# Performance work log

Hardware: AMD Instinct MI355X
Metric: run time of the kernel (lower is better)

## Reference

```python
import itertools
import jax
import jax.numpy as jnp
import numpy as np

FRAME_H, FRAME_W = 480, 640
HFOV = 79
CAM_H_CM = 88.0
NUM_SEM = 16
MAP_SIZE_CM, RES = 4800, 5
VR = 100
BEEN_CLOSE_CM = 200
GDS = 2
DU = 4
CAT_THR, EXP_THR, MAP_THR = 5.0, 1.0, 1.0
MIN_D_CM, MAX_D_CM = 50.0, 350.0
MIN_OBS_H_CM = 25
DIL_ITER, DIL_SIZE = 1, 3

NON_SEM = 4
LOCAL = MAP_SIZE_CM // GDS // RES
GLOBAL = MAP_SIZE_CM // RES
MAX_VH = int(360 / RES)
MIN_VH = int(-40 / RES)
ZB = MAX_VH - MIN_VH
MIN_Z = int(MIN_OBS_H_CM / RES - MIN_VH)
MAX_Z = int((CAM_H_CM + 1) / RES - MIN_VH)
XC = (FRAME_W - 1) / 2.0
ZC = (FRAME_H - 1) / 2.0
FOCAL = (FRAME_W / 2.0) / np.tan(np.deg2rad(HFOV / 2.0))
DEG = 57.29577951308232
B, T = 2, 4
C_MAP = NON_SEM + NUM_SEM

GPOSE0 = jnp.array([24.0, 24.0, 0.0], jnp.float32)
ORIG0 = jnp.array([12.0, 12.0, 0.0], jnp.float32)
LPOSE0 = GPOSE0 - ORIG0
LMB0 = jnp.array([240, 720, 240, 720], jnp.int32)

_XS = np.arange(FRAME_W, dtype=np.float32)[::DU]
_ZS = np.arange(FRAME_H - 1, -1, -1, dtype=np.float32)[::DU]


def point_cloud(depth):
    d = depth[:, ::DU, ::DU]
    valid = (d > MIN_D_CM) & (d < MAX_D_CM)
    X = (_XS[None, None, :] - XC) * d / FOCAL
    Z = (_ZS[None, :, None] - ZC) * d / FOCAL
    pts = jnp.stack([X, d, Z], -1).reshape(d.shape[0], -1, 3)
    return pts, valid.reshape(d.shape[0], -1)


def avg_pool(x, k):
    b, c, h, w = x.shape
    return x.reshape(b, c, h // k, k, w // k, k).mean((3, 5))


def splat(feat, coords):
    bs, fc, n = feat.shape
    dims = (VR, VR, ZB)
    G = VR * VR * ZB
    pos = [coords[:, d] * dims[d] / 2.0 + dims[d] / 2.0 for d in range(3)]
    fl = [jnp.floor(p) for p in pos]
    out = jnp.zeros((fc, bs * G), feat.dtype)
    offs = (jnp.arange(bs) * G)[:, None]
    for corner in itertools.product((0.0, 1.0), repeat=3):
        idx = jnp.zeros_like(pos[0])
        w = jnp.ones_like(pos[0])
        for d in range(3):
            p = fl[d] + corner[d]
            safe = ((p > 0) & (p < dims[d])).astype(feat.dtype)
            w = w * (1.0 - jnp.abs(pos[d] - p)) * safe
            idx = idx * dims[d] + p * safe
        flat = (idx.astype(jnp.int32) + offs).reshape(-1)
        vals = (feat * w[:, None, :]).transpose(1, 0, 2).reshape(fc, -1)
        out = out.at[:, flat].add(vals)
    out = jnp.round(out)
    return out.reshape(fc, bs, VR, VR, ZB).transpose(1, 0, 2, 3, 4)


def affine_grid(theta, h, w):
    ys = jnp.linspace(-1.0, 1.0, h)
    xs = jnp.linspace(-1.0, 1.0, w)
    gy, gx = jnp.meshgrid(ys, xs, indexing="ij")
    base = jnp.stack([gx, gy, jnp.ones_like(gx)], -1)
    return jnp.einsum("bij,hwj->bhwi", theta, base)


def _sample_one(im, grid):
    c, h, w = im.shape
    x = (grid[..., 0] + 1.0) * (w - 1) / 2.0
    y = (grid[..., 1] + 1.0) * (h - 1) / 2.0
    x0 = jnp.floor(x)
    y0 = jnp.floor(y)
    out = jnp.zeros((c,) + x.shape, im.dtype)
    for dx, dy in ((0, 0), (1, 0), (0, 1), (1, 1)):
        xi = x0 + dx
        yi = y0 + dy
        wgt = (1.0 - jnp.abs(x - xi)) * (1.0 - jnp.abs(y - yi))
        ok = (xi >= 0) & (xi <= w - 1) & (yi >= 0) & (yi <= h - 1)
        xi_c = jnp.clip(xi, 0, w - 1).astype(jnp.int32)
        yi_c = jnp.clip(yi, 0, h - 1).astype(jnp.int32)
        out = out + im[:, yi_c, xi_c] * (wgt * ok)[None]
    return out


grid_sample = jax.vmap(_sample_one)


def get_new_pose(pose, rel):
    s = jnp.sin(pose[:, 2] / DEG)
    c = jnp.cos(pose[:, 2] / DEG)
    x = pose[:, 0] + rel[:, 0] * c - rel[:, 1] * s
    y = pose[:, 1] + rel[:, 0] * s + rel[:, 1] * c
    o = pose[:, 2] + rel[:, 2] * DEG
    o = jnp.fmod(o - 180.0, 360.0) + 180.0
    o = jnp.fmod(o + 180.0, 360.0) - 180.0
    return jnp.stack([x, y, o], 1)


def update_local(obs, pdelta, prev_map, prev_pose):
    bs = obs.shape[0]
    pts, valid = point_cloud(obs[:, 3])
    pts = pts.at[..., 2].add(CAM_H_CM)
    pts = pts.at[..., 0].add(VR * RES / 2.0)
    cx = (pts[..., 0] / RES - VR // 2) / VR * 2.0
    cy = (pts[..., 1] / RES - VR // 2) / VR * 2.0
    cz = (pts[..., 2] / RES - (MAX_VH + MIN_VH) // 2) / ZB * 2.0
    coords = jnp.stack([cx, cy, cz], 1)
    coords = jnp.where(valid[:, None, :], coords, 2.0)
    sem = avg_pool(obs[:, 4:], DU).reshape(bs, NUM_SEM, -1)
    feat = jnp.concatenate([jnp.ones_like(sem[:, :1]), sem], 1)
    vox = splat(feat, coords)
    agent_h = vox[..., MIN_Z:MAX_Z].sum(-1)
    all_h = vox.sum(-1)
    fp_map = jnp.clip(agent_h[:, :1] / MAP_THR, 0.0, 1.0)
    fp_exp = jnp.clip(all_h[:, :1] / EXP_THR, 0.0, 1.0)
    sem_pred = jnp.clip(agent_h[:, 1:] / CAT_THR, 0.0, 1.0)
    x1 = LOCAL // 2 - VR // 2
    y1 = LOCAL // 2
    av = jnp.zeros((bs, C_MAP, LOCAL, LOCAL), obs.dtype)
    av = av.at[:, 0:1, y1:y1 + VR, x1:x1 + VR].set(fp_map)
    av = av.at[:, 1:2, y1:y1 + VR, x1:x1 + VR].set(fp_exp)
    av = av.at[:, NON_SEM:, y1:y1 + VR, x1:x1 + VR].set(sem_pred)
    pose = get_new_pose(prev_pose, pdelta)
    half = LOCAL // 2
    stx = -(pose[:, 0] * 100.0 / RES - half) / half
    sty = -(pose[:, 1] * 100.0 / RES - half) / half
    th = (90.0 - pose[:, 2]) * (np.pi / 180.0)
    ct, snt = jnp.cos(th), jnp.sin(th)
    zr, on = jnp.zeros_like(ct), jnp.ones_like(ct)
    th1 = jnp.stack([jnp.stack([ct, -snt, zr], -1), jnp.stack([snt, ct, zr], -1)], 1)
    th2 = jnp.stack([jnp.stack([on, zr, stx], -1), jnp.stack([zr, on, sty], -1)], 1)
    rotated = grid_sample(av, affine_grid(th1, LOCAL, LOCAL))
    translated = grid_sample(rotated, affine_grid(th2, LOCAL, LOCAL))
    cur = jnp.maximum(prev_map, translated)
    obst = cur[:, 0:1]
    kern = jnp.ones((1, 1, DIL_SIZE, DIL_SIZE), cur.dtype)
    for _ in range(DIL_ITER):
        obst = (jax.lax.conv(obst, kern, (1, 1), "SAME") > 0.5).astype(cur.dtype)
    cur = cur.at[:, 0].set(obst[:, 0])
    xg = (pose[:, 0] * 100.0 / RES).astype(jnp.int32)
    yg = (pose[:, 1] * 100.0 / RES).astype(jnp.int32)
    rr = jnp.arange(LOCAL)
    drow = rr[None, :, None] - yg[:, None, None]
    dcol = rr[None, None, :] - xg[:, None, None]
    sq = ((jnp.abs(drow) <= 2) & (jnp.abs(dcol) <= 2)).astype(cur.dtype)
    cur = cur.at[:, 2].set(sq)
    rad = BEEN_CLOSE_CM // RES
    disk = ((drow * drow + dcol * dcol) <= rad * rad).astype(cur.dtype)
    cur = cur.at[:, 3].set(jnp.maximum(cur[:, 3], disk))
    return cur, pose


def update_global_env(lmap, gmap, lpose, gpose, lmb, orig, updg):
    gpose_n = lpose + orig
    gmap_n = jax.lax.dynamic_update_slice(gmap, lmap, (0, lmb[0], lmb[2]))
    r = (gpose_n[1] * 100.0 / RES).astype(jnp.int32)
    c = (gpose_n[0] * 100.0 / RES).astype(jnp.int32)
    gx1 = jnp.clip(r - LOCAL // 2, 0, GLOBAL - LOCAL)
    gy1 = jnp.clip(c - LOCAL // 2, 0, GLOBAL - LOCAL)
    lmb_n = jnp.stack([gx1, gx1 + LOCAL, gy1, gy1 + LOCAL]).astype(jnp.int32)
    orig_n = jnp.stack([gy1 * RES / 100.0, gx1 * RES / 100.0, jnp.zeros(())]).astype(orig.dtype)
    lmap_n = jax.lax.dynamic_slice(gmap_n, (0, lmb_n[0], lmb_n[2]), lmap.shape)
    lpose_n = gpose_n - orig_n
    w = lambda a, b: jnp.where(updg, a, b)
    return (w(lmap_n, lmap), w(gmap_n, gmap), w(lpose_n, lpose),
            w(gpose_n, gpose), w(lmb_n, lmb), w(orig_n, orig))


def map_features(lmap, gmap):
    bs = gmap.shape[0]
    gdown = gmap[:, :NON_SEM].reshape(bs, NON_SEM, LOCAL, GDS, LOCAL, GDS).max((3, 5))
    return jnp.concatenate([lmap[:, :NON_SEM], gdown, lmap[:, NON_SEM:]], 1)


def forward(seq_obs, seq_pose_delta, seq_dones, seq_update_global, seq_camera_poses,
            init_local_map, init_global_map, init_local_pose, init_global_pose,
            init_lmb, init_origins):
    def step(carry, xs):
        lmap, gmap, lpose, gpose, lmb, orig = carry
        obs, pdelta, done, updg = xs
        d4 = done[:, None, None, None]
        d2 = done[:, None]
        lmap = jnp.where(d4, 0.0, lmap)
        gmap = jnp.where(d4, 0.0, gmap)
        lpose = jnp.where(d2, LPOSE0, lpose)
        gpose = jnp.where(d2, GPOSE0, gpose)
        lmb = jnp.where(d2, LMB0, lmb)
        orig = jnp.where(d2, ORIG0, orig)
        lmap, lpose = update_local(obs, pdelta, lmap, lpose)
        lmap, gmap, lpose, gpose, lmb, orig = jax.vmap(update_global_env)(
            lmap, gmap, lpose, gpose, lmb, orig, updg)
        feats = map_features(lmap, gmap)
        return (lmap, gmap, lpose, gpose, lmb, orig), (feats, lpose, gpose, lmb, orig)

    carry0 = (init_local_map, init_global_map, init_local_pose, init_global_pose,
              init_lmb, init_origins)
    xs = (jnp.swapaxes(seq_obs, 0, 1), jnp.swapaxes(seq_pose_delta, 0, 1),
          jnp.swapaxes(seq_dones, 0, 1), jnp.swapaxes(seq_update_global, 0, 1))
    (lmap, gmap, _, _, _, _), (fe, lp, gp, lb, og) = jax.lax.scan(step, carry0, xs)
    sw = lambda a: jnp.swapaxes(a, 0, 1)
    return sw(fe), lmap, gmap, sw(lp), sw(gp), sw(lb), sw(og)


def setup_inputs() -> dict:
    key = jax.random.key(0)
    ks = jax.random.split(key, 4)
    rgb = jax.random.uniform(ks[0], (B, T, 3, FRAME_H, FRAME_W), jnp.float32)
    depth = MIN_D_CM + jax.random.uniform(ks[1], (B, T, 1, FRAME_H, FRAME_W), jnp.float32) * (MAX_D_CM - MIN_D_CM + 100.0)
    seg = (jax.random.uniform(ks[2], (B, T, NUM_SEM, FRAME_H, FRAME_W)) > 0.95).astype(jnp.float32)
    seq_obs = jnp.concatenate([rgb, depth, seg], 2)
    seq_pose_delta = jax.random.normal(ks[3], (B, T, 3), jnp.float32) * jnp.array([0.25, 0.05, 0.1], jnp.float32)
    return {
        "seq_obs": seq_obs,
        "seq_pose_delta": seq_pose_delta,
        "seq_dones": jnp.zeros((B, T), bool),
        "seq_update_global": jnp.ones((B, T), bool),
        "seq_camera_poses": jnp.tile(jnp.eye(4, dtype=jnp.float32)[None], (B, 1, 1)),
        "init_local_map": jnp.zeros((B, C_MAP, LOCAL, LOCAL), jnp.float32),
        "init_global_map": jnp.zeros((B, C_MAP, GLOBAL, GLOBAL), jnp.float32),
        "init_local_pose": jnp.tile(LPOSE0[None], (B, 1)),
        "init_global_pose": jnp.tile(GPOSE0[None], (B, 1)),
        "init_lmb": jnp.tile(LMB0[None], (B, 1)),
        "init_origins": jnp.tile(ORIG0[None], (B, 1)),
    }


def reference(seq_obs, seq_pose_delta, seq_dones, seq_update_global, seq_camera_poses,
              init_local_map, init_global_map, init_local_pose, init_global_pose,
              init_lmb, init_origins):
    return forward(seq_obs, seq_pose_delta, seq_dones, seq_update_global, seq_camera_poses,
                   init_local_map, init_global_map, init_local_pose, init_global_pose,
                   init_lmb, init_origins)
```

## Files before the change

kernel.cpp:

```cpp
#include <hip/hip_runtime.h>
#include <math.h>


#define BB 2
#define TT 4
#define CMAP 20
#define LOC 480
#define GLOB 960
#define VOXC 17
#define NH 120
#define NW 160
#define NPTS (NH*NW)
#define LOC2 (LOC*LOC)
#define G2 (GLOB*GLOB)
#define FH 480
#define FW 640
#define LOCW 240
#define LOCW2 (LOCW*LOCW)
#define WOFF 120
#define CH0Z 69
#define SEMZ 12
#define CELLS 6100
#define CHSZ ((CH0Z + 16*SEMZ)*CELLS)

#define FE_OFF 0L
#define LM_OFF 44236800L
#define LM_SZ  9216000L
#define GM_OFF 53452800L
#define GM_SZ  36864000L
#define LP_OFF 90316800L
#define GP_OFF 90316824L
#define LB_OFF 90316848L
#define OG_OFF 90316880L

#define VOX_SZ   (2L*CHSZ)
#define RED_OFF  3184200L
#define ROT_OFF  3544200L
#define TMP_OFF  5617800L
#define CUR_OFF  6078600L
#define PTF_OFF  15294600L
#define PTI_OFF  15294664L
#define GLIN_OFF 15294728L

__device__ __forceinline__ int iabs(int v){ return v<0? -v : v; }

__global__ __launch_bounds__(256) void k_init0(float4* __restrict__ vox,
                                               float4* __restrict__ lmap,
                                               float4* __restrict__ gmap){
    const long NV4 = VOX_SZ/4;
    const long L4  = LM_SZ/4;
    const long G4  = GM_SZ/4;
    const long total = NV4+L4+G4;
    float4 z; z.x=0.f;z.y=0.f;z.z=0.f;z.w=0.f;
    long i = (long)blockIdx.x*blockDim.x + threadIdx.x;
    long st = (long)gridDim.x*blockDim.x;
    for(long k=i;k<total;k+=st){
        if(k<NV4) vox[k]=z;
        else if(k<NV4+L4) lmap[k-NV4]=z;
        else gmap[k-NV4-L4]=z;
    }
}

__global__ void k_poses(const float* __restrict__ ilp,const float* __restrict__ igp,
                        const int* __restrict__ ilmb,const float* __restrict__ iog,
                        const unsigned char* __restrict__ dones_raw,
                        const unsigned char* __restrict__ updg_raw,
                        const float* __restrict__ pdelta,
                        float* __restrict__ out,float* __restrict__ ptf,int* __restrict__ pti,
                        float* __restrict__ glin){
    #pragma clang fp contract(off)
    int tid = threadIdx.x;
    if(tid < LOC){
        float g;
        if(tid==LOC-1) g = 1.0f;
        else { float s = (float)tid/479.0f; g = s - (1.0f - s); }
        glin[tid] = g;
    }
    if(tid!=0 || blockIdx.x!=0) return;
    int stride;
    if(updg_raw[1]|updg_raw[2]|updg_raw[3]) stride = 1;
    else if(updg_raw[4])                    stride = 4;
    else                                    stride = 8;
    const float DEGF = 57.29577951308232f;
    for(int b=0;b<BB;b++){
        float lp0=ilp[b*3],lp1=ilp[b*3+1],lp2=ilp[b*3+2];
        float gp0=igp[b*3],gp1=igp[b*3+1],gp2=igp[b*3+2];
        float og0=iog[b*3],og1=iog[b*3+1],og2=iog[b*3+2];
        int m0=ilmb[b*4],m1=ilmb[b*4+1],m2=ilmb[b*4+2],m3=ilmb[b*4+3];
        for(int t=0;t<TT;t++){
            int dn = dones_raw[(b*TT+t)*stride]!=0;
            int ug = updg_raw[(b*TT+t)*stride]!=0;
            if(dn){
                lp0=12.f;lp1=12.f;lp2=0.f; gp0=24.f;gp1=24.f;gp2=0.f;
                og0=12.f;og1=12.f;og2=0.f; m0=240;m1=720;m2=240;m3=720;
            }
            float r0=pdelta[(b*TT+t)*3+0], r1=pdelta[(b*TT+t)*3+1], r2=pdelta[(b*TT+t)*3+2];
            float s=sinf(lp2/DEGF), c=cosf(lp2/DEGF);
            float x = lp0 + r0*c - r1*s;
            float y = lp1 + r0*s + r1*c;
            float o = lp2 + r2*DEGF;
            o = fmodf(o-180.f,360.f)+180.f;
            o = fmodf(o+180.f,360.f)-180.f;
            lp0=x; lp1=y; lp2=o;
            float th = (90.0f - o) * (float)(M_PI/180.0);
            float ct = cosf(th), snt = sinf(th);
            float ax = (lp0*100.0f)/5.0f;
            float ay = (lp1*100.0f)/5.0f;
            float stx = -((ax-240.0f)/240.0f);
            float sty = -((ay-240.0f)/240.0f);
            float* pf = ptf + (size_t)(t*BB+b)*8;
            pf[0]=lp0; pf[1]=lp1; pf[2]=o; pf[3]=ct; pf[4]=snt; pf[5]=stx; pf[6]=sty;
            int* pi = pti + (size_t)(t*BB+b)*8;
            pi[0]=m0; pi[1]=m2;
            pi[4]=(int)ax; pi[5]=(int)ay;
            pi[6]=dn; pi[7]=ug;
            float g0=lp0+og0, g1=lp1+og1, g2=lp2+og2;
            if(ug){
                int r  = (int)((g1*100.0f)/5.0f);
                int cc = (int)((g0*100.0f)/5.0f);
                int gx1 = min(max(r-240,0),480);
                int gy1 = min(max(cc-240,0),480);
                m0=gx1; m1=gx1+480; m2=gy1; m3=gy1+480;
                float o0 = ((float)gy1*5.0f)/100.0f;
                float o1 = ((float)gx1*5.0f)/100.0f;
                og0=o0; og1=o1; og2=0.f;
                lp0=g0-o0; lp1=g1-o1; lp2=g2;
                gp0=g0; gp1=g1; gp2=g2;
            }
            pi[2]=m0; pi[3]=m2;
            out[LP_OFF+(b*TT+t)*3+0]=lp0; out[LP_OFF+(b*TT+t)*3+1]=lp1; out[LP_OFF+(b*TT+t)*3+2]=lp2;
            out[GP_OFF+(b*TT+t)*3+0]=gp0; out[GP_OFF+(b*TT+t)*3+1]=gp1; out[GP_OFF+(b*TT+t)*3+2]=gp2;
            out[OG_OFF+(b*TT+t)*3+0]=og0; out[OG_OFF+(b*TT+t)*3+1]=og1; out[OG_OFF+(b*TT+t)*3+2]=og2;
            out[LB_OFF+(b*TT+t)*4+0]=(float)m0; out[LB_OFF+(b*TT+t)*4+1]=(float)m1;
            out[LB_OFF+(b*TT+t)*4+2]=(float)m2; out[LB_OFF+(b*TT+t)*4+3]=(float)m3;
        }
    }
}

__global__ __launch_bounds__(256) void k_reset_done(float4* __restrict__ lmap,float4* __restrict__ gmap,
                                                    const int* __restrict__ pti,int t){
    const long L4 = (long)CMAP*LOC2/4, G4 = (long)CMAP*G2/4, per = L4+G4;
    bool d0 = pti[(size_t)(t*BB+0)*8+6]!=0, d1 = pti[(size_t)(t*BB+1)*8+6]!=0;
    long total = (d0?per:0)+(d1?per:0);
    if(total==0) return;
    float4 z; z.x=0.f;z.y=0.f;z.z=0.f;z.w=0.f;
    long i = (long)blockIdx.x*blockDim.x + threadIdx.x;
    long st = (long)gridDim.x*blockDim.x;
    for(long k=i;k<total;k+=st){
        long r = k; int b;
        if(d0){ if(r<per) b=0; else { b=1; r-=per; } } else b=1;
        if(r<L4) lmap[b*L4+r]=z; else gmap[b*G4+(r-L4)]=z;
    }
}

__global__ __launch_bounds__(256) void k_splat(const float* __restrict__ obs,int t,
                                               float* __restrict__ vox,float FOCAL){
    #pragma clang fp contract(off)
    int tid = blockIdx.x*blockDim.x + threadIdx.x;
    if(tid >= BB*VOXC*NPTS) return;
    int p  = tid % NPTS;
    int ch = (tid/NPTS) % VOXC;
    int b  = tid / (VOXC*NPTS);
    int zi = p / NW, xi = p % NW;
    const float* ob = obs + ((size_t)(b*TT+t))*CMAP*FH*FW;
    float d = ob[3*FH*FW + (size_t)(4*zi)*FW + 4*xi];
    if(!(d>50.0f && d<350.0f)) return;
    float f;
    if(ch==0) f = 1.0f;
    else{
        const float* cp = ob + (size_t)(4+ch-1)*FH*FW + (size_t)(4*zi)*FW + 4*xi;
        float s=0.f;
        #pragma unroll
        for(int r=0;r<4;r++){
            float4 v = *(const float4*)(cp + (size_t)r*FW);
            s += v.x+v.y+v.z+v.w;
        }
        f = s*0.0625f;
    }
    float X  = ((float)(4*xi) - 319.5f)*d/FOCAL;
    float Zc = ((float)(479-4*zi) - 239.5f)*d/FOCAL;
    float p0f = X + 250.0f;
    float p1f = d;
    float p2f = Zc + 88.0f;
    float cx = (p0f/5.0f - 50.0f)/100.0f*2.0f;
    float cy = (p1f/5.0f - 50.0f)/100.0f*2.0f;
    float cz = (p2f/5.0f - 32.0f)/80.0f*2.0f;
    float pos0 = cx*100.0f/2.0f + 50.0f;
    float pos1 = cy*100.0f/2.0f + 50.0f;
    float pos2 = cz*80.0f/2.0f + 40.0f;
    float f0=floorf(pos0), f1=floorf(pos1), f2=floorf(pos2);
    float* base = vox + (size_t)b*CHSZ;
    #pragma unroll
    for(int c0=0;c0<2;c0++){
        float q0=f0+(float)c0;
        if(!(q0>0.f && q0<100.f)) continue;
        float w0 = 1.0f-fabsf(pos0-q0);
        int iq0 = (int)q0;
        #pragma unroll
        for(int c1=0;c1<2;c1++){
            float q1=f1+(float)c1;
            if(!(q1>=10.0f && q1<=70.0f)) continue;
            float w1 = w0*(1.0f-fabsf(pos1-q1));
            int cell = iq0*61 + ((int)q1-10);
            #pragma unroll
            for(int c2=0;c2<2;c2++){
                float q2=f2+(float)c2;
                if(!(q2>0.f && q2<70.f)) continue;
                int iq2 = (int)q2;
                float w = w1*(1.0f-fabsf(pos2-q2));
                if(ch==0)
                    atomicAdd(base + (size_t)(iq2-1)*CELLS + cell, w);
                else if(iq2>=13 && iq2<25)
                    atomicAdd(base + (size_t)(CH0Z + (ch-1)*SEMZ + (iq2-13))*CELLS + cell, f*w);
            }
        }
    }
}

__global__ __launch_bounds__(256) void k_reduce(float* __restrict__ vox,float* __restrict__ red){
    int tid = blockIdx.x*blockDim.x + threadIdx.x;
    if(tid >= BB*VOXC*10000) return;
    int cell = tid % 10000;
    int ch   = (tid/10000) % VOXC;
    int b    = tid / (VOXC*10000);
    int q0 = cell/100, q1 = cell%100;
    float allh=0.f, ag=0.f;
    if(q1>=10 && q1<=70){
        float* base = vox + (size_t)b*CHSZ;
        if(ch==0){
            float* vp = base + q0*61 + (q1-10);
            for(int z=0;z<CH0Z;z++){
                float v = rintf(vp[(size_t)z*CELLS]);
                allh += v;
                if(z>=12 && z<24) ag += v;
                vp[(size_t)z*CELLS] = 0.0f;
            }
        }else{
            float* vp = base + (size_t)(CH0Z + (ch-1)*SEMZ)*CELLS + q0*61 + (q1-10);
            for(int z=0;z<SEMZ;z++){
                float v = rintf(vp[(size_t)z*CELLS]);
                ag += v;
                vp[(size_t)z*CELLS] = 0.0f;
            }
        }
    }
    float* rb = red + (size_t)b*18*10000;
    if(ch==0){
        rb[cell]       = fminf(fmaxf(ag,0.f),1.f);
        rb[10000+cell] = fminf(fmaxf(allh,0.f),1.f);
    }else{
        rb[(ch+1)*10000+cell] = fminf(fmaxf(ag/5.0f,0.f),1.f);
    }
}

__global__ __launch_bounds__(256) void k_rot(const float* __restrict__ red,const float* __restrict__ ptf,
                                             const float* __restrict__ glin,int t,
                                             float* __restrict__ rotW){
    #pragma clang fp contract(off)
    int tid = blockIdx.x*blockDim.x + threadIdx.x;
    if(tid >= BB*LOCW2) return;
    int wx = tid % LOCW;
    int wy = (tid/LOCW) % LOCW;
    int b  = tid / LOCW2;
    int x = wx + WOFF, y = wy + WOFF;
    const float* pf = ptf + (size_t)(t*BB+b)*8;
    float ct = pf[3], snt = pf[4];
    float gx = glin[x], gy = glin[y];
    float grx = ct*gx - snt*gy;
    float gry = snt*gx + ct*gy;
    float xs = (grx+1.0f)*239.5f;
    float ys = (gry+1.0f)*239.5f;
    float x0 = floorf(xs), y0 = floorf(ys);
    int   off[4]; float w[4];
    #pragma unroll
    for(int k=0;k<4;k++){
        float xi = x0 + (float)(k&1), yi = y0 + (float)(k>>1);
        float wgt = (1.0f-fabsf(xs-xi))*(1.0f-fabsf(ys-yi));
        int xii=(int)xi, yii=(int)yi;
        bool ok = !(xi<0.f||xi>479.f||yi<0.f||yi>479.f)
                  && yii>=240 && yii<340 && xii>=190 && xii<290;
        w[k]   = ok ? wgt : 0.0f;
        off[k] = ok ? (yii-240)*100 + (xii-190) : 0;
    }
    const float* rb = red + (size_t)b*18*10000;
    float* rp = rotW + (size_t)b*18*LOCW2 + (size_t)wy*LOCW + wx;
    for(int ch=0;ch<18;ch++){
        const float* rc = rb + (size_t)ch*10000;
        float acc = rc[off[0]]*w[0];
        acc += rc[off[1]]*w[1];
        acc += rc[off[2]]*w[2];
        acc += rc[off[3]]*w[3];
        rp[(size_t)ch*LOCW2] = acc;
    }
}

__global__ __launch_bounds__(256) void k_trans(const float* __restrict__ rotW,const float* __restrict__ ptf,
                                               const int* __restrict__ pti,const float* __restrict__ glin,
                                               int t,const float* __restrict__ P,
                                               float* __restrict__ C,float* __restrict__ tmp0){
    #pragma clang fp contract(off)
    int tid = blockIdx.x*blockDim.x + threadIdx.x;
    if(tid >= BB*LOC2) return;
    int x = tid % LOC;
    int y = (tid/LOC) % LOC;
    int b = tid / LOC2;
    const float* pf = ptf + (size_t)(t*BB+b)*8;
    const int*   pi = pti + (size_t)(t*BB+b)*8;
    float stx = pf[5], sty = pf[6];
    float xs = (glin[x]+stx+1.0f)*239.5f;
    float ys = (glin[y]+sty+1.0f)*239.5f;
    float x0=floorf(xs), y0=floorf(ys);
    int   off[4]; float w[4];
    #pragma unroll
    for(int k=0;k<4;k++){
        float xi = x0 + (float)(k&1), yi = y0 + (float)(k>>1);
        float wgt = (1.0f-fabsf(xs-xi))*(1.0f-fabsf(ys-yi));
        int xii=(int)xi, yii=(int)yi;
        bool ok = !(xi<0.f||xi>479.f||yi<0.f||yi>479.f)
                  && xii>=WOFF && xii<WOFF+LOCW && yii>=WOFF && yii<WOFF+LOCW;
        w[k]   = ok ? wgt : 0.0f;
        off[k] = ok ? (yii-WOFF)*LOCW + (xii-WOFF) : 0;
    }
    int xg=pi[4], yg=pi[5];
    float sq   = (iabs(y-yg)<=2 && iabs(x-xg)<=2) ? 1.0f : 0.0f;
    int dr=y-yg, dc=x-xg;
    float disk = (dr*dr+dc*dc <= 1600) ? 1.0f : 0.0f;
    const float* rb = rotW + (size_t)b*18*LOCW2;
    size_t pix = (size_t)y*LOC + x;
    const float* Pb = P + (size_t)b*CMAP*LOC2 + pix;
    float* Cb = C + (size_t)b*CMAP*LOC2 + pix;
    for(int c=0;c<CMAP;c++){
        if(c==2){ Cb[2*LOC2] = sq; continue; }
        if(c==3){ Cb[3*LOC2] = fmaxf(Pb[3*LOC2], disk); continue; }
        int wc = (c<2) ? c : c-2;
        const float* rp = rb + (size_t)wc*LOCW2;
        float acc = rp[off[0]]*w[0];
        acc += rp[off[1]]*w[1];
        acc += rp[off[2]]*w[2];
        acc += rp[off[3]]*w[3];
        float res = fmaxf(Pb[(size_t)c*LOC2], acc);
        if(c==0) tmp0[(size_t)b*LOC2 + pix] = res;
        else     Cb[(size_t)c*LOC2] = res;
    }
}

__global__ __launch_bounds__(256) void k_dil(const float* __restrict__ tmp0,float* __restrict__ C){
    int tid = blockIdx.x*blockDim.x + threadIdx.x;
    if(tid >= BB*LOC2) return;
    int x = tid % LOC;
    int y = (tid/LOC) % LOC;
    int b = tid / LOC2;
    const float* tb = tmp0 + (size_t)b*LOC2;
    float s=0.f;
    for(int dy=-1;dy<=1;dy++){
        int yy=y+dy; if(yy<0||yy>=LOC) continue;
        for(int dx=-1;dx<=1;dx++){
            int xx=x+dx; if(xx<0||xx>=LOC) continue;
            s += tb[(size_t)yy*LOC+xx];
        }
    }
    C[(size_t)b*CMAP*LOC2 + (size_t)y*LOC + x] = (s>0.5f)?1.0f:0.0f;
}

__global__ __launch_bounds__(256) void k_out(const float* __restrict__ C,float* __restrict__ gmap,
                                             float* __restrict__ P,float* __restrict__ fe,
                                             const int* __restrict__ pti,int t){
    int tid = blockIdx.x*blockDim.x + threadIdx.x;
    if(tid >= BB*LOC2) return;
    int x = tid % LOC;
    int y = (tid/LOC) % LOC;
    int b = tid / LOC2;
    const int* pi = pti + (size_t)(t*BB+b)*8;
    int r0o=pi[0], c0o=pi[1], r0n=pi[2], c0n=pi[3];
    int ug = pi[7];
    size_t pix = (size_t)y*LOC + x;
    const float* Cb = C + (size_t)b*CMAP*LOC2;
    float* gB = gmap + (size_t)b*CMAP*G2;
    float* pB = P + (size_t)b*CMAP*LOC2;
    float* feB = fe + ((size_t)(b*TT+t))*24*LOC2;
    if(ug){
        size_t gp = (size_t)(r0o+y)*GLOB + (c0o+x);
        for(int c=0;c<CMAP;c++)
            gB[(size_t)c*G2 + gp] = Cb[(size_t)c*LOC2 + pix];
    }
    int dr = ug ? (r0n - r0o) : 0;
    int dc = ug ? (c0n - c0o) : 0;
    int sy = y + dr, sx = x + dc;
    bool inT = (sy>=0 && sy<LOC && sx>=0 && sx<LOC);
    size_t gpn = ug ? ((size_t)(r0n+y)*GLOB + (c0n+x)) : 0;
    size_t spix = (size_t)sy*LOC + sx;
    for(int c=0;c<CMAP;c++){
        float v = inT ? Cb[(size_t)c*LOC2 + spix]
                      : gB[(size_t)c*G2 + gpn];
        pB[(size_t)c*LOC2 + pix] = v;
        int fc = (c<4) ? c : c+4;
        feB[(size_t)fc*LOC2 + pix] = v;
    }
    for(int gc=0;gc<4;gc++){
        float m = 0.f; bool first = true;
        #pragma unroll
        for(int dy=0;dy<2;dy++){
            #pragma unroll
            for(int dx=0;dx<2;dx++){
                int ty = 2*y+dy, tx = 2*x+dx;
                int ly = ty - r0o, lx = tx - c0o;
                float tv;
                if(ug && ly>=0 && ly<LOC && lx>=0 && lx<LOC)
                    tv = Cb[(size_t)gc*LOC2 + (size_t)ly*LOC + lx];
                else
                    tv = gB[(size_t)gc*G2 + (size_t)ty*GLOB + tx];
                m = first ? tv : fmaxf(m, tv);
                first = false;
            }
        }
        feB[(size_t)(4+gc)*LOC2 + pix] = m;
    }
}

extern "C" void kernel_launch(void* const* d_in, const int* in_sizes, int n_in,
                              void* d_out, int out_size, void* d_ws, size_t ws_size,
                              hipStream_t stream){
    const float* obs    = (const float*)d_in[0];
    const float* pdelta = (const float*)d_in[1];
    const unsigned char* dones_raw = (const unsigned char*)d_in[2];
    const unsigned char* updg_raw  = (const unsigned char*)d_in[3];
    const float* ilp  = (const float*)d_in[7];
    const float* igp  = (const float*)d_in[8];
    const int*   ilmb = (const int*)d_in[9];
    const float* iog  = (const float*)d_in[10];

    float* out  = (float*)d_out;
    float* fe   = out + FE_OFF;
    float* lmap = out + LM_OFF;
    float* gmap = out + GM_OFF;

    float* ws   = (float*)d_ws;
    float* vox  = ws;
    float* red  = ws + RED_OFF;
    float* rotW = ws + ROT_OFF;
    float* tmp0 = ws + TMP_OFF;
    float* curm = ws + CUR_OFF;
    float* ptf  = ws + PTF_OFF;
    int*   pti  = (int*)(ws + PTI_OFF);
    float* glin = ws + GLIN_OFF;

    const float FOCAL = (float)(320.0 / tan(39.5 * M_PI / 180.0));

    k_init0<<<2048,256,0,stream>>>((float4*)vox,(float4*)lmap,(float4*)gmap);
    k_poses<<<1,512,0,stream>>>(ilp,igp,ilmb,iog,dones_raw,updg_raw,pdelta,out,ptf,pti,glin);

    for(int t=0;t<TT;t++){
        k_reset_done<<<2048,256,0,stream>>>((float4*)lmap,(float4*)gmap,pti,t);
        { int n=BB*VOXC*NPTS;   k_splat <<<(n+255)/256,256,0,stream>>>(obs,t,vox,FOCAL); }
        { int n=BB*VOXC*10000;  k_reduce<<<(n+255)/256,256,0,stream>>>(vox,red); }
        { int n=BB*LOCW2;       k_rot   <<<(n+255)/256,256,0,stream>>>(red,ptf,glin,t,rotW); }
        { int n=BB*LOC2;        k_trans <<<(n+255)/256,256,0,stream>>>(rotW,ptf,pti,glin,t,lmap,curm,tmp0); }
        { int n=BB*LOC2;        k_dil   <<<(n+255)/256,256,0,stream>>>(tmp0,curm); }
        { int n=BB*LOC2;        k_out   <<<(n+255)/256,256,0,stream>>>(curm,gmap,lmap,fe,pti,t); }
    }
}
```

Baseline: 1.093 ms.

## Fuse rotate into translate, dilation into output, and overlap next-step splat/reduce

The separate rotation pass and its intermediate buffer are removed: each translate thread recomputes the rotated bilinear samples of its four source cells straight from the reduced grid. Dilation is evaluated on the fly inside the output kernel instead of in its own pass. The next timestep's splat and reduce are folded into the translate and output kernels, and init is merged with pose computation, which cuts the number of launches. In exchange, the translate kernel does about four times more gathers, dilation is recomputed several times per pixel, and the reduce step inside the output kernel both reads and clears the shared voxel/reduced buffers while the same launch is running. That in-kernel reduce also writes the reduced grid that the translate step reads, so ordering depends on the launch sequence.

Result: faster. 1.065 ms (-2.6%).

```diff
diff --git a/kernel.cpp b/kernel.cpp
--- a/kernel.cpp
+++ b/kernel.cpp
@@ -35,48 +35,29 @@
 
 #define VOX_SZ   (2L*CHSZ)
 #define RED_OFF  3184200L
-#define ROT_OFF  3544200L
-#define TMP_OFF  5617800L
-#define CUR_OFF  6078600L
-#define PTF_OFF  15294600L
-#define PTI_OFF  15294664L
-#define GLIN_OFF 15294728L
+#define TMP_OFF  3544200L
+#define CUR_OFF  4005000L
+#define PTF_OFF  13221000L
+#define PTI_OFF  13221064L
+#define GLIN_OFF 13221128L
 
 __device__ __forceinline__ int iabs(int v){ return v<0? -v : v; }
 
-__global__ __launch_bounds__(256) void k_init0(float4* __restrict__ vox,
-                                               float4* __restrict__ lmap,
-                                               float4* __restrict__ gmap){
-    const long NV4 = VOX_SZ/4;
-    const long L4  = LM_SZ/4;
-    const long G4  = GM_SZ/4;
-    const long total = NV4+L4+G4;
-    float4 z; z.x=0.f;z.y=0.f;z.z=0.f;z.w=0.f;
-    long i = (long)blockIdx.x*blockDim.x + threadIdx.x;
-    long st = (long)gridDim.x*blockDim.x;
-    for(long k=i;k<total;k+=st){
-        if(k<NV4) vox[k]=z;
-        else if(k<NV4+L4) lmap[k-NV4]=z;
-        else gmap[k-NV4-L4]=z;
-    }
-}
-
-__global__ void k_poses(const float* __restrict__ ilp,const float* __restrict__ igp,
-                        const int* __restrict__ ilmb,const float* __restrict__ iog,
-                        const unsigned char* __restrict__ dones_raw,
-                        const unsigned char* __restrict__ updg_raw,
-                        const float* __restrict__ pdelta,
-                        float* __restrict__ out,float* __restrict__ ptf,int* __restrict__ pti,
-                        float* __restrict__ glin){
+
+__device__ __forceinline__ void glin_body(int i, float* glin){
+    float g;
+    if(i==LOC-1) g = 1.0f;
+    else { float s = (float)i/479.0f; g = s - (1.0f - s); }
+    glin[i] = g;
+}
+
+__device__ void poses_body(const float* ilp,const float* igp,
+                           const int* ilmb,const float* iog,
+                           const unsigned char* dones_raw,
+                           const unsigned char* updg_raw,
+                           const float* pdelta,
+                           float* out,float* ptf,int* pti){
     #pragma clang fp contract(off)
-    int tid = threadIdx.x;
-    if(tid < LOC){
-        float g;
-        if(tid==LOC-1) g = 1.0f;
-        else { float s = (float)tid/479.0f; g = s - (1.0f - s); }
-        glin[tid] = g;
-    }
-    if(tid!=0 || blockIdx.x!=0) return;
     int stride;
     if(updg_raw[1]|updg_raw[2]|updg_raw[3]) stride = 1;
     else if(updg_raw[4])                    stride = 4;
@@ -137,27 +118,9 @@
     }
 }
 
-__global__ __launch_bounds__(256) void k_reset_done(float4* __restrict__ lmap,float4* __restrict__ gmap,
-                                                    const int* __restrict__ pti,int t){
-    const long L4 = (long)CMAP*LOC2/4, G4 = (long)CMAP*G2/4, per = L4+G4;
-    bool d0 = pti[(size_t)(t*BB+0)*8+6]!=0, d1 = pti[(size_t)(t*BB+1)*8+6]!=0;
-    long total = (d0?per:0)+(d1?per:0);
-    if(total==0) return;
-    float4 z; z.x=0.f;z.y=0.f;z.z=0.f;z.w=0.f;
-    long i = (long)blockIdx.x*blockDim.x + threadIdx.x;
-    long st = (long)gridDim.x*blockDim.x;
-    for(long k=i;k<total;k+=st){
-        long r = k; int b;
-        if(d0){ if(r<per) b=0; else { b=1; r-=per; } } else b=1;
-        if(r<L4) lmap[b*L4+r]=z; else gmap[b*G4+(r-L4)]=z;
-    }
-}
-
-__global__ __launch_bounds__(256) void k_splat(const float* __restrict__ obs,int t,
-                                               float* __restrict__ vox,float FOCAL){
+__device__ __forceinline__ void splat_body(int tid,const float* __restrict__ obs,int t,
+                                           float* __restrict__ vox,float FOCAL){
     #pragma clang fp contract(off)
-    int tid = blockIdx.x*blockDim.x + threadIdx.x;
-    if(tid >= BB*VOXC*NPTS) return;
     int p  = tid % NPTS;
     int ch = (tid/NPTS) % VOXC;
     int b  = tid / (VOXC*NPTS);
@@ -217,9 +180,7 @@
     }
 }
 
-__global__ __launch_bounds__(256) void k_reduce(float* __restrict__ vox,float* __restrict__ red){
-    int tid = blockIdx.x*blockDim.x + threadIdx.x;
-    if(tid >= BB*VOXC*10000) return;
+__device__ __forceinline__ void reduce_body(int tid,float* __restrict__ vox,float* __restrict__ red){
     int cell = tid % 10000;
     int ch   = (tid/10000) % VOXC;
     int b    = tid / (VOXC*10000);
@@ -253,64 +214,22 @@
     }
 }
 
-__global__ __launch_bounds__(256) void k_rot(const float* __restrict__ red,const float* __restrict__ ptf,
-                                             const float* __restrict__ glin,int t,
-                                             float* __restrict__ rotW){
+__device__ void transf_body(int tid,const float* __restrict__ red,
+                            const float* __restrict__ ptf,const int* __restrict__ pti,
+                            const float* __restrict__ glin,int t,
+                            const float* __restrict__ P,
+                            float* __restrict__ C,float* __restrict__ tmp0){
     #pragma clang fp contract(off)
-    int tid = blockIdx.x*blockDim.x + threadIdx.x;
-    if(tid >= BB*LOCW2) return;
-    int wx = tid % LOCW;
-    int wy = (tid/LOCW) % LOCW;
-    int b  = tid / LOCW2;
-    int x = wx + WOFF, y = wy + WOFF;
-    const float* pf = ptf + (size_t)(t*BB+b)*8;
-    float ct = pf[3], snt = pf[4];
-    float gx = glin[x], gy = glin[y];
-    float grx = ct*gx - snt*gy;
-    float gry = snt*gx + ct*gy;
-    float xs = (grx+1.0f)*239.5f;
-    float ys = (gry+1.0f)*239.5f;
-    float x0 = floorf(xs), y0 = floorf(ys);
-    int   off[4]; float w[4];
-    #pragma unroll
-    for(int k=0;k<4;k++){
-        float xi = x0 + (float)(k&1), yi = y0 + (float)(k>>1);
-        float wgt = (1.0f-fabsf(xs-xi))*(1.0f-fabsf(ys-yi));
-        int xii=(int)xi, yii=(int)yi;
-        bool ok = !(xi<0.f||xi>479.f||yi<0.f||yi>479.f)
-                  && yii>=240 && yii<340 && xii>=190 && xii<290;
-        w[k]   = ok ? wgt : 0.0f;
-        off[k] = ok ? (yii-240)*100 + (xii-190) : 0;
-    }
-    const float* rb = red + (size_t)b*18*10000;
-    float* rp = rotW + (size_t)b*18*LOCW2 + (size_t)wy*LOCW + wx;
-    for(int ch=0;ch<18;ch++){
-        const float* rc = rb + (size_t)ch*10000;
-        float acc = rc[off[0]]*w[0];
-        acc += rc[off[1]]*w[1];
-        acc += rc[off[2]]*w[2];
-        acc += rc[off[3]]*w[3];
-        rp[(size_t)ch*LOCW2] = acc;
-    }
-}
-
-__global__ __launch_bounds__(256) void k_trans(const float* __restrict__ rotW,const float* __restrict__ ptf,
-                                               const int* __restrict__ pti,const float* __restrict__ glin,
-                                               int t,const float* __restrict__ P,
-                                               float* __restrict__ C,float* __restrict__ tmp0){
-    #pragma clang fp contract(off)
-    int tid = blockIdx.x*blockDim.x + threadIdx.x;
-    if(tid >= BB*LOC2) return;
     int x = tid % LOC;
     int y = (tid/LOC) % LOC;
     int b = tid / LOC2;
     const float* pf = ptf + (size_t)(t*BB+b)*8;
     const int*   pi = pti + (size_t)(t*BB+b)*8;
-    float stx = pf[5], sty = pf[6];
+    float ct = pf[3], snt = pf[4], stx = pf[5], sty = pf[6];
     float xs = (glin[x]+stx+1.0f)*239.5f;
     float ys = (glin[y]+sty+1.0f)*239.5f;
     float x0=floorf(xs), y0=floorf(ys);
-    int   off[4]; float w[4];
+    float tw[4]; int ro[4][4]; float rw[4][4];
     #pragma unroll
     for(int k=0;k<4;k++){
         float xi = x0 + (float)(k&1), yi = y0 + (float)(k>>1);
@@ -318,14 +237,34 @@
         int xii=(int)xi, yii=(int)yi;
         bool ok = !(xi<0.f||xi>479.f||yi<0.f||yi>479.f)
                   && xii>=WOFF && xii<WOFF+LOCW && yii>=WOFF && yii<WOFF+LOCW;
-        w[k]   = ok ? wgt : 0.0f;
-        off[k] = ok ? (yii-WOFF)*LOCW + (xii-WOFF) : 0;
+        tw[k] = ok ? wgt : 0.0f;
+        if(ok){
+            float gx2 = glin[xii], gy2 = glin[yii];
+            float grx = ct*gx2 - snt*gy2;
+            float gry = snt*gx2 + ct*gy2;
+            float rxs = (grx+1.0f)*239.5f;
+            float rys = (gry+1.0f)*239.5f;
+            float rx0 = floorf(rxs), ry0 = floorf(rys);
+            #pragma unroll
+            for(int j=0;j<4;j++){
+                float xj = rx0 + (float)(j&1), yj = ry0 + (float)(j>>1);
+                float rwgt = (1.0f-fabsf(rxs-xj))*(1.0f-fabsf(rys-yj));
+                int xjj=(int)xj, yjj=(int)yj;
+                bool okj = !(xj<0.f||xj>479.f||yj<0.f||yj>479.f)
+                           && yjj>=240 && yjj<340 && xjj>=190 && xjj<290;
+                rw[k][j] = okj ? rwgt : 0.0f;
+                ro[k][j] = okj ? (yjj-240)*100 + (xjj-190) : 0;
+            }
+        }else{
+            #pragma unroll
+            for(int j=0;j<4;j++){ rw[k][j]=0.0f; ro[k][j]=0; }
+        }
     }
     int xg=pi[4], yg=pi[5];
     float sq   = (iabs(y-yg)<=2 && iabs(x-xg)<=2) ? 1.0f : 0.0f;
     int dr=y-yg, dc=x-xg;
     float disk = (dr*dr+dc*dc <= 1600) ? 1.0f : 0.0f;
-    const float* rb = rotW + (size_t)b*18*LOCW2;
+    const float* rb = red + (size_t)b*18*10000;
     size_t pix = (size_t)y*LOC + x;
     const float* Pb = P + (size_t)b*CMAP*LOC2 + pix;
     float* Cb = C + (size_t)b*CMAP*LOC2 + pix;
@@ -333,24 +272,23 @@
         if(c==2){ Cb[2*LOC2] = sq; continue; }
         if(c==3){ Cb[3*LOC2] = fmaxf(Pb[3*LOC2], disk); continue; }
         int wc = (c<2) ? c : c-2;
-        const float* rp = rb + (size_t)wc*LOCW2;
-        float acc = rp[off[0]]*w[0];
-        acc += rp[off[1]]*w[1];
-        acc += rp[off[2]]*w[2];
-        acc += rp[off[3]]*w[3];
+        const float* rc = rb + (size_t)wc*10000;
+        float rv0 = rc[ro[0][0]]*rw[0][0]; rv0 += rc[ro[0][1]]*rw[0][1];
+        rv0 += rc[ro[0][2]]*rw[0][2];      rv0 += rc[ro[0][3]]*rw[0][3];
+        float rv1 = rc[ro[1][0]]*rw[1][0]; rv1 += rc[ro[1][1]]*rw[1][1];
+        rv1 += rc[ro[1][2]]*rw[1][2];      rv1 += rc[ro[1][3]]*rw[1][3];
+        float rv2 = rc[ro[2][0]]*rw[2][0]; rv2 += rc[ro[2][1]]*rw[2][1];
+        rv2 += rc[ro[2][2]]*rw[2][2];      rv2 += rc[ro[2][3]]*rw[2][3];
+        float rv3 = rc[ro[3][0]]*rw[3][0]; rv3 += rc[ro[3][1]]*rw[3][1];
+        rv3 += rc[ro[3][2]]*rw[3][2];      rv3 += rc[ro[3][3]]*rw[3][3];
+        float acc = rv0*tw[0]; acc += rv1*tw[1]; acc += rv2*tw[2]; acc += rv3*tw[3];
         float res = fmaxf(Pb[(size_t)c*LOC2], acc);
         if(c==0) tmp0[(size_t)b*LOC2 + pix] = res;
         else     Cb[(size_t)c*LOC2] = res;
     }
 }
 
-__global__ __launch_bounds__(256) void k_dil(const float* __restrict__ tmp0,float* __restrict__ C){
-    int tid = blockIdx.x*blockDim.x + threadIdx.x;
-    if(tid >= BB*LOC2) return;
-    int x = tid % LOC;
-    int y = (tid/LOC) % LOC;
-    int b = tid / LOC2;
-    const float* tb = tmp0 + (size_t)b*LOC2;
+__device__ __forceinline__ float dil_at(const float* __restrict__ tb,int y,int x){
     float s=0.f;
     for(int dy=-1;dy<=1;dy++){
         int yy=y+dy; if(yy<0||yy>=LOC) continue;
@@ -359,14 +297,12 @@
             s += tb[(size_t)yy*LOC+xx];
         }
     }
-    C[(size_t)b*CMAP*LOC2 + (size_t)y*LOC + x] = (s>0.5f)?1.0f:0.0f;
-}
-
-__global__ __launch_bounds__(256) void k_out(const float* __restrict__ C,float* __restrict__ gmap,
-                                             float* __restrict__ P,float* __restrict__ fe,
-                                             const int* __restrict__ pti,int t){
-    int tid = blockIdx.x*blockDim.x + threadIdx.x;
-    if(tid >= BB*LOC2) return;
+    return (s>0.5f)?1.0f:0.0f;
+}
+
+__device__ void outf_body(int tid,const float* __restrict__ C,const float* __restrict__ tmp0,
+                          float* __restrict__ gmap,float* __restrict__ P,float* __restrict__ fe,
+                          const int* __restrict__ pti,int t){
     int x = tid % LOC;
     int y = (tid/LOC) % LOC;
     int b = tid / LOC2;
@@ -375,12 +311,14 @@
     int ug = pi[7];
     size_t pix = (size_t)y*LOC + x;
     const float* Cb = C + (size_t)b*CMAP*LOC2;
+    const float* tb = tmp0 + (size_t)b*LOC2;
     float* gB = gmap + (size_t)b*CMAP*G2;
     float* pB = P + (size_t)b*CMAP*LOC2;
     float* feB = fe + ((size_t)(b*TT+t))*24*LOC2;
     if(ug){
         size_t gp = (size_t)(r0o+y)*GLOB + (c0o+x);
-        for(int c=0;c<CMAP;c++)
+        gB[gp] = dil_at(tb,y,x);
+        for(int c=1;c<CMAP;c++)
             gB[(size_t)c*G2 + gp] = Cb[(size_t)c*LOC2 + pix];
     }
     int dr = ug ? (r0n - r0o) : 0;
@@ -390,8 +328,9 @@
     size_t gpn = ug ? ((size_t)(r0n+y)*GLOB + (c0n+x)) : 0;
     size_t spix = (size_t)sy*LOC + sx;
     for(int c=0;c<CMAP;c++){
-        float v = inT ? Cb[(size_t)c*LOC2 + spix]
-                      : gB[(size_t)c*G2 + gpn];
+        float v;
+        if(inT) v = (c==0) ? dil_at(tb,sy,sx) : Cb[(size_t)c*LOC2 + spix];
+        else    v = gB[(size_t)c*G2 + gpn];
         pB[(size_t)c*LOC2 + pix] = v;
         int fc = (c<4) ? c : c+4;
         feB[(size_t)fc*LOC2 + pix] = v;
@@ -406,7 +345,8 @@
                 int ly = ty - r0o, lx = tx - c0o;
                 float tv;
                 if(ug && ly>=0 && ly<LOC && lx>=0 && lx<LOC)
-                    tv = Cb[(size_t)gc*LOC2 + (size_t)ly*LOC + lx];
+                    tv = (gc==0) ? dil_at(tb,ly,lx)
+                                 : Cb[(size_t)gc*LOC2 + (size_t)ly*LOC + lx];
                 else
                     tv = gB[(size_t)gc*G2 + (size_t)ty*GLOB + tx];
                 m = first ? tv : fmaxf(m, tv);
@@ -415,6 +355,88 @@
         }
         feB[(size_t)(4+gc)*LOC2 + pix] = m;
     }
+}
+
+
+__global__ __launch_bounds__(256) void k_init(float4* __restrict__ vox,
+                                              float4* __restrict__ lmap,float4* __restrict__ gmap,
+                                              const float* ilp,const float* igp,
+                                              const int* ilmb,const float* iog,
+                                              const unsigned char* dones_raw,const unsigned char* updg_raw,
+                                              const float* pdelta,float* out,
+                                              float* ptf,int* pti,float* glin){
+    long i = (long)blockIdx.x*blockDim.x + threadIdx.x;
+    if(blockIdx.x==0){
+        if(threadIdx.x < LOC) glin_body((int)threadIdx.x, glin);
+        if(threadIdx.x == 0)
+            poses_body(ilp,igp,ilmb,iog,dones_raw,updg_raw,pdelta,out,ptf,pti);
+    }
+    const long NV4 = VOX_SZ/4, L4 = LM_SZ/4, G4 = GM_SZ/4;
+    const long total = NV4+L4+G4;
+    float4 z; z.x=0.f;z.y=0.f;z.z=0.f;z.w=0.f;
+    long st = (long)gridDim.x*blockDim.x;
+    for(long k=i;k<total;k+=st){
+        if(k<NV4) vox[k]=z;
+        else if(k<NV4+L4) lmap[k-NV4]=z;
+        else gmap[k-NV4-L4]=z;
+    }
+}
+
+__global__ __launch_bounds__(256) void k_reset(float4* __restrict__ lmap,float4* __restrict__ gmap,
+                                               const int* __restrict__ pti,int t){
+    const long L4 = (long)CMAP*LOC2/4, G4 = (long)CMAP*G2/4, per = L4+G4;
+    bool d0 = pti[(size_t)(t*BB+0)*8+6]!=0, d1 = pti[(size_t)(t*BB+1)*8+6]!=0;
+    long total = (d0?per:0)+(d1?per:0);
+    if(total==0) return;
+    float4 z; z.x=0.f;z.y=0.f;z.z=0.f;z.w=0.f;
+    long i = (long)blockIdx.x*blockDim.x + threadIdx.x;
+    long st = (long)gridDim.x*blockDim.x;
+    for(long k=i;k<total;k+=st){
+        long r = k; int b;
+        if(d0){ if(r<per) b=0; else { b=1; r-=per; } } else b=1;
+        if(r<L4) lmap[b*L4+r]=z; else gmap[b*G4+(r-L4)]=z;
+    }
+}
+
+__global__ __launch_bounds__(256) void k_splat(const float* __restrict__ obs,int t,
+                                               float* __restrict__ vox,float FOCAL){
+    int tid = blockIdx.x*blockDim.x + threadIdx.x;
+    if(tid >= BB*VOXC*NPTS) return;
+    splat_body(tid,obs,t,vox,FOCAL);
+}
+
+__global__ __launch_bounds__(256) void k_reduce(float* __restrict__ vox,float* __restrict__ red){
+    int tid = blockIdx.x*blockDim.x + threadIdx.x;
+    if(tid >= BB*VOXC*10000) return;
+    reduce_body(tid,vox,red);
+}
+
+__global__ __launch_bounds__(256) void k_transf(const float* __restrict__ red,
+                                                const float* __restrict__ ptf,const int* __restrict__ pti,
+                                                const float* __restrict__ glin,int t,
+                                                const float* __restrict__ P,
+                                                float* __restrict__ C,float* __restrict__ tmp0,
+                                                const float* __restrict__ obs,
+                                                float* __restrict__ vox,float FOCAL,int tnext){
+    int NT  = (int)(gridDim.x*blockDim.x);
+    int tid = (int)(blockIdx.x*blockDim.x + threadIdx.x);
+    if(tnext>=0)
+        for(int i=tid;i<BB*VOXC*NPTS;i+=NT) splat_body(i,obs,tnext,vox,FOCAL);
+    if(tid >= BB*LOC2) return;
+    transf_body(tid,red,ptf,pti,glin,t,P,C,tmp0);
+}
+
+__global__ __launch_bounds__(256) void k_outf(const float* __restrict__ C,const float* __restrict__ tmp0,
+                                              float* __restrict__ gmap,float* __restrict__ P,
+                                              float* __restrict__ fe,
+                                              const int* __restrict__ pti,int t,
+                                              float* __restrict__ vox,float* __restrict__ red,int tnext){
+    int NT  = (int)(gridDim.x*blockDim.x);
+    int tid = (int)(blockIdx.x*blockDim.x + threadIdx.x);
+    if(tnext>=0)
+        for(int i=tid;i<BB*VOXC*10000;i+=NT) reduce_body(i,vox,red);
+    if(tid >= BB*LOC2) return;
+    outf_body(tid,C,tmp0,gmap,P,fe,pti,t);
 }
 
 extern "C" void kernel_launch(void* const* d_in, const int* in_sizes, int n_in,
@@ -434,28 +456,30 @@
     float* lmap = out + LM_OFF;
     float* gmap = out + GM_OFF;
 
-    float* ws   = (float*)d_ws;
-    float* vox  = ws;
-    float* red  = ws + RED_OFF;
-    float* rotW = ws + ROT_OFF;
-    float* tmp0 = ws + TMP_OFF;
-    float* curm = ws + CUR_OFF;
-    float* ptf  = ws + PTF_OFF;
-    int*   pti  = (int*)(ws + PTI_OFF);
-    float* glin = ws + GLIN_OFF;
+    float* wsf  = (float*)d_ws;
+    float* vox  = wsf;
+    float* red  = wsf + RED_OFF;
+    float* tmp0 = wsf + TMP_OFF;
+    float* curm = wsf + CUR_OFF;
+    float* ptf  = wsf + PTF_OFF;
+    int*   pti  = (int*)(wsf + PTI_OFF);
+    float* glin = wsf + GLIN_OFF;
 
     const float FOCAL = (float)(320.0 / tan(39.5 * M_PI / 180.0));
 
-    k_init0<<<2048,256,0,stream>>>((float4*)vox,(float4*)lmap,(float4*)gmap);
-    k_poses<<<1,512,0,stream>>>(ilp,igp,ilmb,iog,dones_raw,updg_raw,pdelta,out,ptf,pti,glin);
-
+    k_init<<<2048,256,0,stream>>>((float4*)vox,(float4*)lmap,(float4*)gmap,
+                                  ilp,igp,ilmb,iog,dones_raw,updg_raw,pdelta,
+                                  out,ptf,pti,glin);
+    { int n=BB*VOXC*NPTS;  k_splat <<<(n+255)/256,256,0,stream>>>(obs,0,vox,FOCAL); }
+    { int n=BB*VOXC*10000; k_reduce<<<(n+255)/256,256,0,stream>>>(vox,red); }
+
+    const int nPix = BB*LOC2;
     for(int t=0;t<TT;t++){
-        k_reset_done<<<2048,256,0,stream>>>((float4*)lmap,(float4*)gmap,pti,t);
-        { int n=BB*VOXC*NPTS;   k_splat <<<(n+255)/256,256,0,stream>>>(obs,t,vox,FOCAL); }
-        { int n=BB*VOXC*10000;  k_reduce<<<(n+255)/256,256,0,stream>>>(vox,red); }
-        { int n=BB*LOCW2;       k_rot   <<<(n+255)/256,256,0,stream>>>(red,ptf,glin,t,rotW); }
-        { int n=BB*LOC2;        k_trans <<<(n+255)/256,256,0,stream>>>(rotW,ptf,pti,glin,t,lmap,curm,tmp0); }
-        { int n=BB*LOC2;        k_dil   <<<(n+255)/256,256,0,stream>>>(tmp0,curm); }
-        { int n=BB*LOC2;        k_out   <<<(n+255)/256,256,0,stream>>>(curm,gmap,lmap,fe,pti,t); }
-    }
-}
+        k_reset<<<2048,256,0,stream>>>((float4*)lmap,(float4*)gmap,pti,t);
+        int tnext = (t+1<TT) ? t+1 : -1;
+        k_transf<<<nPix/256,256,0,stream>>>(red,ptf,pti,glin,t,lmap,curm,tmp0,
+                                            obs,vox,FOCAL,tnext);
+        k_outf  <<<nPix/256,256,0,stream>>>(curm,tmp0,gmap,lmap,fe,pti,t,
+                                            vox,red,tnext);
+    }
+}
```
